# Performance work log

Hardware: AMD Instinct MI355X
Metric: run time of the kernel (lower is better)

The kernel has to match this reference:

```python
import jax, jax.numpy as jnp
import numpy as np

# Module config (init_kwargs)
CIN, COUT, KH, KW = 256, 256, 3, 3
STRIDE, PADDING = 1, 1
T = 64                 # psum chunk size along the reduction (K) axis
NBITS = 8              # saturating accumulator bits (signed)
QMAX = (1 << (NBITS - 1)) - 1   # 127
QMIN = QMAX - (1 << NBITS) + 1  # -128


def setup_inputs() -> dict:
    key = jax.random.key(0)
    k1, k2 = jax.random.split(key)
    x = jax.random.normal(k1, (8, CIN, 56, 56), dtype=jnp.float32)
    # nn.Parameter(torch.rand((N,1)) * 0.001)
    weights = jax.random.uniform(k2, (CIN * COUT * KH * KW, 1), dtype=jnp.float32) * 0.001
    return {"x": x, "weights": weights}


def reference(x, weights):
    B, _, H, W = x.shape
    OH = (H - KH + 2 * PADDING) // STRIDE + 1
    OW = (W - KW + 2 * PADDING) // STRIDE + 1

    w = weights.reshape(COUT, CIN, KH, KW)
    # per-output-channel scaling factor, detached
    scale = jax.lax.stop_gradient(jnp.mean(jnp.abs(w), axis=(1, 2, 3), keepdims=True))
    # binarize with STE: sign(w).detach() - clamp(w).detach() + clamp(w)
    wc = jnp.clip(w, -1.0, 1.0)
    wb = jax.lax.stop_gradient(jnp.sign(w) - wc) + wc

    # unfold (im2col); channel varies slowest -> matches torch.nn.functional.unfold
    patches = jax.lax.conv_general_dilated_patches(
        x, (KH, KW), (STRIDE, STRIDE), [(PADDING, PADDING), (PADDING, PADDING)]
    )  # [B, CIN*KH*KW, OH*OW... (spatial)]
    K = CIN * KH * KW
    L = OH * OW
    A = patches.reshape(B, K, L).transpose(0, 2, 1)  # [B, L, K]
    X = wb.reshape(COUT, K).T                        # [K, COUT]

    pad = (-K) % T
    if pad:
        A = jnp.pad(A, ((0, 0), (0, 0), (0, pad)))
        X = jnp.pad(X, ((0, pad), (0, 0)))
    nT = (K + pad) // T

    A4 = A.reshape(B, L, nT, T)        # chunked reduction axis
    X3 = X.reshape(nT, T, COUT)
    # per-chunk partial sums (satmm_cuda.forward_psum)
    psum = jnp.einsum('blnt,ntc->nblc', A4, X3)  # [nT, B, L, COUT]

    # saturating sequential accumulation: reduce(lambda a,b: clip(a+b, QMIN, QMAX))
    def step(carry, p):
        return jnp.clip(carry + p, QMIN, QMAX), None
    y_flat, _ = jax.lax.scan(step, psum[0], psum[1:])  # [B, L, COUT]

    y = y_flat.transpose(0, 2, 1).reshape(B, COUT, OH, OW)
    y = y * scale.reshape(1, -1, 1, 1)
    # psum returned in the original [B, L, COUT, nT] layout
    return y, psum.transpose(1, 2, 3, 0)
```

## Files before the change

kernel.cpp:

```cpp
#include <hip/hip_runtime.h>
#include <hip/hip_bf16.h>

#define CIN 256
#define COUT 256
#define HW 56
#define BATCH 8
#define L_SPATIAL 3136
#define K_TOTAL 2304
#define NT 36
#define KSTRIDE 2312
#define ATILE_BYTES (16 * KSTRIDE * 2)
#define STAGE_FLOATS 2304
#define LDS_BYTES (ATILE_BYTES + 8 * STAGE_FLOATS * 4)
#define QMAXF 127.0f
#define QMINF -128.0f

typedef short bf16x8 __attribute__((ext_vector_type(8)));
typedef float f32x4 __attribute__((ext_vector_type(4)));

__global__ __launch_bounds__(256) void prep_kernel(
    const float* __restrict__ w, unsigned short* __restrict__ bsign,
    float* __restrict__ scale) {
  const int c = blockIdx.x;
  const int t = threadIdx.x;
  const float* row = w + (size_t)c * K_TOTAL;
  unsigned short* out = bsign + (size_t)c * K_TOTAL;
  float acc = 0.0f;
#pragma unroll
  for (int j = 0; j < 9; ++j) {
    const int k = t + 256 * j;
    const float v = row[k];
    acc += __builtin_fabsf(v);
    out[k] = (v > 0.0f) ? (unsigned short)0x3F80
           : ((v < 0.0f) ? (unsigned short)0xBF80 : (unsigned short)0);
  }
#pragma unroll
  for (int o = 32; o > 0; o >>= 1) acc += __shfl_down(acc, o, 64);
  __shared__ float red[4];
  if ((t & 63) == 0) red[t >> 6] = acc;
  __syncthreads();
  if (t == 0) scale[c] = (red[0] + red[1] + red[2] + red[3]) * (1.0f / 2304.0f);
}

__global__ __launch_bounds__(512, 1) void satconv_kernel(
    const float* __restrict__ x, const unsigned short* __restrict__ bsign,
    const float* __restrict__ scale, float* __restrict__ y_out,
    float* __restrict__ psum_out) {
  extern __shared__ char smem[];
  unsigned short* Atile = (unsigned short*)smem;
  float* stage_base = (float*)(smem + ATILE_BYTES);

  const int tid = threadIdx.x;
  const int m0 = blockIdx.x << 4;

  {
    const int ml = tid & 15;
    const int grp = tid >> 4;
    const int m = m0 + ml;
    const int b = m / L_SPATIAL;
    const int l = m - b * L_SPATIAL;
    const int oh = l / HW;
    const int ow = l - oh * HW;
    const float* xb = x + (size_t)b * (CIN * L_SPATIAL);
    unsigned short* arow = Atile + ml * KSTRIDE;
    for (int r = grp; r < 768; r += 32) {
      const int ci = r / 3;
      const int kh = r - ci * 3;
      const int h = oh + kh - 1;
      const bool hv = ((unsigned)h < (unsigned)HW);
      const float* xr = xb + (ci * HW + h) * HW;
      const int kb = ci * 9 + kh * 3;
#pragma unroll
      for (int kw = 0; kw < 3; ++kw) {
        const int wv = ow + kw - 1;
        float v = 0.0f;
        if (hv && ((unsigned)wv < (unsigned)HW)) v = xr[wv];
        __hip_bfloat16 bv = __float2bfloat16(v);
        arow[kb + kw] = *reinterpret_cast<unsigned short*>(&bv);
      }
    }
  }
  __syncthreads();

  const int lane = tid & 63;
  const int wave = tid >> 6;
  const int cl = lane & 15;
  const int q = lane >> 4;
  const int c0 = wave << 5;
  float* stage = stage_base + wave * STAGE_FLOATS;

  const unsigned short* aptr = Atile + cl * KSTRIDE + q * 8;
  const int b_img = m0 / L_SPATIAL;
  const int l0 = m0 - b_img * L_SPATIAL;

  for (int s = 0; s < 2; ++s) {
    const int csub0 = c0 + (s << 4);
    const int c = csub0 + cl;
    const unsigned short* bptr = bsign + (size_t)c * K_TOTAL + q * 8;
    f32x4 ps[NT];
    f32x4 sacc = {0.0f, 0.0f, 0.0f, 0.0f};
    const f32x4 zero = {0.0f, 0.0f, 0.0f, 0.0f};
#pragma unroll
    for (int n = 0; n < NT; ++n) {
      bf16x8 a0 = *reinterpret_cast<const bf16x8*>(aptr + n * 64);
      bf16x8 a1 = *reinterpret_cast<const bf16x8*>(aptr + n * 64 + 32);
      bf16x8 b0 = *reinterpret_cast<const bf16x8*>(bptr + n * 64);
      bf16x8 b1 = *reinterpret_cast<const bf16x8*>(bptr + n * 64 + 32);
      f32x4 acc = __builtin_amdgcn_mfma_f32_16x16x32_bf16(a0, b0, zero, 0, 0, 0);
      acc = __builtin_amdgcn_mfma_f32_16x16x32_bf16(a1, b1, acc, 0, 0, 0);
      ps[n] = acc;
      if (n == 0) {
        sacc = acc;
      } else {
#pragma unroll
        for (int e = 0; e < 4; ++e) {
          const float t = sacc[e] + acc[e];
          sacc[e] = __builtin_amdgcn_fmed3f(t, QMINF, QMAXF);
        }
      }
    }

#pragma unroll
    for (int rg = 0; rg < 4; ++rg) {
#pragma unroll
      for (int g = 0; g < 9; ++g) {
        f32x4 v = {ps[4 * g + 0][rg], ps[4 * g + 1][rg],
                   ps[4 * g + 2][rg], ps[4 * g + 3][rg]};
        *reinterpret_cast<f32x4*>(stage + q * 576 + cl * 36 + 4 * g) = v;
      }
#pragma unroll
      for (int it = 0; it < 9; ++it) {
        const int f = it * 256 + lane * 4;
        const int qq = f / 576;
        const int rem = f - qq * 576;
        const int ci = rem / 36;
        const int n0 = rem - ci * 36;
        f32x4 v = *reinterpret_cast<const f32x4*>(stage + f);
        const size_t goff =
            ((size_t)(m0 + (qq << 2) + rg) * COUT + (csub0 + ci)) * NT + n0;
        *reinterpret_cast<f32x4*>(psum_out + goff) = v;
      }
    }

    {
      const float sc = scale[c];
      f32x4 yv;
#pragma unroll
      for (int e = 0; e < 4; ++e) yv[e] = sacc[e] * sc;
      *reinterpret_cast<f32x4*>(stage + cl * 16 + q * 4) = yv;
      const int ci = lane >> 2;
      const int mi = (lane & 3) << 2;
      f32x4 v = *reinterpret_cast<const f32x4*>(stage + lane * 4);
      *reinterpret_cast<f32x4*>(
          y_out + ((size_t)b_img * COUT + (csub0 + ci)) * L_SPATIAL + l0 + mi) = v;
    }
  }
}

extern "C" void kernel_launch(void* const* d_in, const int* in_sizes, int n_in,
                              void* d_out, int out_size, void* d_ws, size_t ws_size,
                              hipStream_t stream) {
  const float* x = (const float*)d_in[0];
  const float* w = (const float*)d_in[1];
  float* y = (float*)d_out;
  float* psum = y + (size_t)BATCH * COUT * L_SPATIAL;
  unsigned short* bsign = (unsigned short*)d_ws;
  float* scale = (float*)((char*)d_ws + (size_t)COUT * K_TOTAL * 2);

  prep_kernel<<<COUT, 256, 0, stream>>>(w, bsign, scale);

  hipFuncSetAttribute(reinterpret_cast<const void*>(satconv_kernel),
                      hipFuncAttributeMaxDynamicSharedMemorySize, LDS_BYTES);
  satconv_kernel<<<(BATCH * L_SPATIAL) / 16, 512, LDS_BYTES, stream>>>(
      x, bsign, scale, y, psum);
}
```

Before: 1.259 ms.

## Persistent conv kernel with bit-packed sign weights and prefetched im2col tiles

Replaces the one-block-per-tile launch with a persistent grid of 224 blocks, each processing 7 tiles. The next tile's im2col gather is prefetched into registers while the current tile computes. Weights are stored as sign and zero bitplanes that are expanded into bf16 ±1 fragments in registers, which removes most of the weight-fragment loads from global memory. It also swizzles the A tile layout in LDS, pads the psum staging buffer, and allows two blocks per CU. The cost is higher register pressure from holding two 36-entry accumulator arrays plus the prefetch buffer, and more complex barrier handling.

Result: slower. 2.136 ms (+69.6%).

```diff
diff --git a/kernel.cpp b/kernel.cpp
--- a/kernel.cpp
+++ b/kernel.cpp
@@ -8,152 +8,297 @@
 #define L_SPATIAL 3136
 #define K_TOTAL 2304
 #define NT 36
-#define KSTRIDE 2312
-#define ATILE_BYTES (16 * KSTRIDE * 2)
-#define STAGE_FLOATS 2304
-#define LDS_BYTES (ATILE_BYTES + 8 * STAGE_FLOATS * 4)
+#define TILES_PER_IMG 196
+#define GRID 224
+#define TPW 7
+#define A_U16 36864
+#define STAGE_DW 2340
+#define LDS_BYTES (A_U16 * 2 + 8 * STAGE_DW * 4)
+#define BB_STRIDE 40
+#define ZPLANE (256 * 4 * BB_STRIDE)
 #define QMAXF 127.0f
 #define QMINF -128.0f
 
 typedef short bf16x8 __attribute__((ext_vector_type(8)));
 typedef float f32x4 __attribute__((ext_vector_type(4)));
+typedef unsigned int u32x4 __attribute__((ext_vector_type(4)));
 
 __global__ __launch_bounds__(256) void prep_kernel(
-    const float* __restrict__ w, unsigned short* __restrict__ bsign,
+    const float* __restrict__ w, unsigned short* __restrict__ bbits,
     float* __restrict__ scale) {
   const int c = blockIdx.x;
   const int t = threadIdx.x;
   const float* row = w + (size_t)c * K_TOTAL;
-  unsigned short* out = bsign + (size_t)c * K_TOTAL;
-  float acc = 0.0f;
-#pragma unroll
-  for (int j = 0; j < 9; ++j) {
-    const int k = t + 256 * j;
-    const float v = row[k];
-    acc += __builtin_fabsf(v);
-    out[k] = (v > 0.0f) ? (unsigned short)0x3F80
-           : ((v < 0.0f) ? (unsigned short)0xBF80 : (unsigned short)0);
-  }
+  float acc = 0.f;
+#pragma unroll
+  for (int j = 0; j < 9; ++j) acc += __builtin_fabsf(row[t + 256 * j]);
 #pragma unroll
   for (int o = 32; o > 0; o >>= 1) acc += __shfl_down(acc, o, 64);
   __shared__ float red[4];
   if ((t & 63) == 0) red[t >> 6] = acc;
   __syncthreads();
-  if (t == 0) scale[c] = (red[0] + red[1] + red[2] + red[3]) * (1.0f / 2304.0f);
-}
-
-__global__ __launch_bounds__(512, 1) void satconv_kernel(
-    const float* __restrict__ x, const unsigned short* __restrict__ bsign,
+  if (t == 0) scale[c] = (red[0] + red[1] + red[2] + red[3]) * (1.f / 2304.f);
+  if (t < 144) {
+    const int q = t / 36, n = t - q * 36;
+    unsigned int sbits = 0, zbits = 0;
+#pragma unroll
+    for (int j = 0; j < 8; ++j) {
+      const float v0 = row[n * 64 + q * 8 + j];
+      const float v1 = row[n * 64 + 32 + q * 8 + j];
+      if (v0 < 0.f) sbits |= (1u << j);
+      if (v1 < 0.f) sbits |= (1u << (8 + j));
+      if (v0 == 0.f) zbits |= (1u << j);
+      if (v1 == 0.f) zbits |= (1u << (8 + j));
+    }
+    bbits[(c * 4 + q) * BB_STRIDE + n] = (unsigned short)sbits;
+    bbits[ZPLANE + (c * 4 + q) * BB_STRIDE + n] = (unsigned short)zbits;
+  }
+}
+
+__device__ __forceinline__ void expand_frags(unsigned int t, bf16x8& b0, bf16x8& b1) {
+  u32x4 w0, w1;
+#pragma unroll
+  for (int d = 0; d < 4; ++d) {
+    w0[d] = 0x3F803F80u | ((t & (1u << (2 * d)))     << (15 - 2 * d))
+                        | ((t & (1u << (2 * d + 1))) << (30 - 2 * d));
+    w1[d] = 0x3F803F80u | ((t & (1u << (8 + 2 * d))) << (7 - 2 * d))
+                        | ((t & (1u << (9 + 2 * d))) << (22 - 2 * d));
+  }
+  b0 = __builtin_bit_cast(bf16x8, w0);
+  b1 = __builtin_bit_cast(bf16x8, w1);
+}
+
+template <bool Z>
+__device__ __forceinline__ void run_k(const unsigned short* __restrict__ abase,
+                                      const unsigned int* __restrict__ bb,
+                                      const unsigned int* __restrict__ zb,
+                                      f32x4* __restrict__ ps, f32x4& sacc) {
+  const f32x4 zero = {0.f, 0.f, 0.f, 0.f};
+#pragma unroll
+  for (int n = 0; n < NT; ++n) {
+    const unsigned int td = bb[n >> 1];
+    const unsigned int tb = (n & 1) ? (td >> 16) : (td & 0xFFFFu);
+    bf16x8 b0, b1;
+    expand_frags(tb, b0, b1);
+    if (Z) {
+      const unsigned int zd = zb[n >> 1];
+      const unsigned int zt = (n & 1) ? (zd >> 16) : (zd & 0xFFFFu);
+      if (zt) {
+        u32x4 w0 = __builtin_bit_cast(u32x4, b0);
+        u32x4 w1 = __builtin_bit_cast(u32x4, b1);
+#pragma unroll
+        for (int d = 0; d < 4; ++d) {
+          if (zt & (1u << (2 * d)))     w0[d] &= 0xFFFF0000u;
+          if (zt & (1u << (2 * d + 1))) w0[d] &= 0x0000FFFFu;
+          if (zt & (1u << (8 + 2 * d))) w1[d] &= 0xFFFF0000u;
+          if (zt & (1u << (9 + 2 * d))) w1[d] &= 0x0000FFFFu;
+        }
+        b0 = __builtin_bit_cast(bf16x8, w0);
+        b1 = __builtin_bit_cast(bf16x8, w1);
+      }
+    }
+    bf16x8 a0 = *reinterpret_cast<const bf16x8*>(abase + n * 1024);
+    bf16x8 a1 = *reinterpret_cast<const bf16x8*>(abase + n * 1024 + 512);
+    f32x4 acc = __builtin_amdgcn_mfma_f32_16x16x32_bf16(a0, b0, zero, 0, 0, 0);
+    acc = __builtin_amdgcn_mfma_f32_16x16x32_bf16(a1, b1, acc, 0, 0, 0);
+    ps[n] = acc;
+    if (n == 0) sacc = acc;
+    else {
+#pragma unroll
+      for (int e = 0; e < 4; ++e) {
+        const float tv = sacc[e] + acc[e];
+        sacc[e] = __builtin_amdgcn_fmed3f(tv, QMINF, QMAXF);
+      }
+    }
+  }
+}
+
+__global__ __launch_bounds__(512, 2) void satconv_kernel(
+    const float* __restrict__ x, const unsigned short* __restrict__ bbits,
     const float* __restrict__ scale, float* __restrict__ y_out,
     float* __restrict__ psum_out) {
   extern __shared__ char smem[];
   unsigned short* Atile = (unsigned short*)smem;
-  float* stage_base = (float*)(smem + ATILE_BYTES);
+  float* stage_base = (float*)(smem + A_U16 * 2);
 
   const int tid = threadIdx.x;
-  const int m0 = blockIdx.x << 4;
-
-  {
-    const int ml = tid & 15;
-    const int grp = tid >> 4;
-    const int m = m0 + ml;
-    const int b = m / L_SPATIAL;
-    const int l = m - b * L_SPATIAL;
-    const int oh = l / HW;
-    const int ow = l - oh * HW;
-    const float* xb = x + (size_t)b * (CIN * L_SPATIAL);
-    unsigned short* arow = Atile + ml * KSTRIDE;
-    for (int r = grp; r < 768; r += 32) {
-      const int ci = r / 3;
-      const int kh = r - ci * 3;
-      const int h = oh + kh - 1;
-      const bool hv = ((unsigned)h < (unsigned)HW);
-      const float* xr = xb + (ci * HW + h) * HW;
-      const int kb = ci * 9 + kh * 3;
-#pragma unroll
-      for (int kw = 0; kw < 3; ++kw) {
-        const int wv = ow + kw - 1;
-        float v = 0.0f;
-        if (hv && ((unsigned)wv < (unsigned)HW)) v = xr[wv];
-        __hip_bfloat16 bv = __float2bfloat16(v);
-        arow[kb + kw] = *reinterpret_cast<unsigned short*>(&bv);
-      }
-    }
-  }
-  __syncthreads();
-
   const int lane = tid & 63;
   const int wave = tid >> 6;
   const int cl = lane & 15;
   const int q = lane >> 4;
   const int c0 = wave << 5;
-  float* stage = stage_base + wave * STAGE_FLOATS;
-
-  const unsigned short* aptr = Atile + cl * KSTRIDE + q * 8;
-  const int b_img = m0 / L_SPATIAL;
-  const int l0 = m0 - b_img * L_SPATIAL;
-
-  for (int s = 0; s < 2; ++s) {
-    const int csub0 = c0 + (s << 4);
-    const int c = csub0 + cl;
-    const unsigned short* bptr = bsign + (size_t)c * K_TOTAL + q * 8;
-    f32x4 ps[NT];
-    f32x4 sacc = {0.0f, 0.0f, 0.0f, 0.0f};
-    const f32x4 zero = {0.0f, 0.0f, 0.0f, 0.0f};
-#pragma unroll
-    for (int n = 0; n < NT; ++n) {
-      bf16x8 a0 = *reinterpret_cast<const bf16x8*>(aptr + n * 64);
-      bf16x8 a1 = *reinterpret_cast<const bf16x8*>(aptr + n * 64 + 32);
-      bf16x8 b0 = *reinterpret_cast<const bf16x8*>(bptr + n * 64);
-      bf16x8 b1 = *reinterpret_cast<const bf16x8*>(bptr + n * 64 + 32);
-      f32x4 acc = __builtin_amdgcn_mfma_f32_16x16x32_bf16(a0, b0, zero, 0, 0, 0);
-      acc = __builtin_amdgcn_mfma_f32_16x16x32_bf16(a1, b1, acc, 0, 0, 0);
-      ps[n] = acc;
-      if (n == 0) {
-        sacc = acc;
-      } else {
-#pragma unroll
-        for (int e = 0; e < 4; ++e) {
-          const float t = sacc[e] + acc[e];
-          sacc[e] = __builtin_amdgcn_fmed3f(t, QMINF, QMAXF);
-        }
-      }
-    }
-
-#pragma unroll
-    for (int rg = 0; rg < 4; ++rg) {
-#pragma unroll
-      for (int g = 0; g < 9; ++g) {
-        f32x4 v = {ps[4 * g + 0][rg], ps[4 * g + 1][rg],
-                   ps[4 * g + 2][rg], ps[4 * g + 3][rg]};
-        *reinterpret_cast<f32x4*>(stage + q * 576 + cl * 36 + 4 * g) = v;
-      }
-#pragma unroll
-      for (int it = 0; it < 9; ++it) {
-        const int f = it * 256 + lane * 4;
-        const int qq = f / 576;
-        const int rem = f - qq * 576;
-        const int ci = rem / 36;
-        const int n0 = rem - ci * 36;
-        f32x4 v = *reinterpret_cast<const f32x4*>(stage + f);
-        const size_t goff =
-            ((size_t)(m0 + (qq << 2) + rg) * COUT + (csub0 + ci)) * NT + n0;
-        *reinterpret_cast<f32x4*>(psum_out + goff) = v;
-      }
-    }
-
-    {
-      const float sc = scale[c];
+  float* stage = stage_base + wave * STAGE_DW;
+  const int w_id = blockIdx.x;
+
+  auto load_bb = [&](const unsigned short* plane, int s, unsigned int* bb) {
+    const unsigned short* bp = plane + (size_t)((c0 + (s << 4) + cl) * 4 + q) * BB_STRIDE;
+    const uint4* p4 = (const uint4*)bp;
+    uint4 v0 = p4[0], v1 = p4[1], v2 = p4[2], v3 = p4[3];
+    uint2 v4 = *(const uint2*)(bp + 32);
+    bb[0]=v0.x; bb[1]=v0.y; bb[2]=v0.z; bb[3]=v0.w;
+    bb[4]=v1.x; bb[5]=v1.y; bb[6]=v1.z; bb[7]=v1.w;
+    bb[8]=v2.x; bb[9]=v2.y; bb[10]=v2.z; bb[11]=v2.w;
+    bb[12]=v3.x; bb[13]=v3.y; bb[14]=v3.z; bb[15]=v3.w;
+    bb[16]=v4.x; bb[17]=v4.y;
+  };
+
+  auto load_pack = [&](int m0n, unsigned int* apack) {
+    const int ml = tid & 15;
+    const int grp = tid >> 4;
+    const int m = m0n + ml;
+    const int b = m / L_SPATIAL;
+    const int l = m - b * L_SPATIAL;
+    const int oh = l / HW, ow = l - oh * HW;
+    const float* xb = x + (size_t)b * (CIN * L_SPATIAL);
+#pragma unroll
+    for (int j = 0; j < 24; ++j) {
+      const int r = grp + 32 * j;
+      const int ci = r / 3, kh = r - ci * 3;
+      const int h = oh + kh - 1;
+      const bool hv = ((unsigned)h < (unsigned)HW);
+      const float* xr = xb + (ci * HW + h) * HW;
+#pragma unroll
+      for (int kw = 0; kw < 3; ++kw) {
+        const int wv = ow + kw - 1;
+        float v = 0.f;
+        if (hv && ((unsigned)wv < (unsigned)HW)) v = xr[wv];
+        __hip_bfloat16 bv = __float2bfloat16(v);
+        unsigned int u = (unsigned int)*reinterpret_cast<unsigned short*>(&bv);
+        const int idx = j * 3 + kw;
+        if (idx & 1) apack[idx >> 1] |= (u << 16);
+        else         apack[idx >> 1] = u;
+      }
+    }
+  };
+
+  auto unpack_write = [&](const unsigned int* apack) {
+    const int ml = tid & 15;
+    const int grp = tid >> 4;
+#pragma unroll
+    for (int j = 0; j < 24; ++j) {
+      const int r = grp + 32 * j;
+      const int ci = r / 3, kh = r - ci * 3;
+      const int kb = ci * 9 + kh * 3;
+#pragma unroll
+      for (int kw = 0; kw < 3; ++kw) {
+        const int idx = j * 3 + kw;
+        unsigned int u = apack[idx >> 1];
+        u = (idx & 1) ? (u >> 16) : (u & 0xFFFFu);
+        const int k = kb + kw;
+        const int addr = ((k >> 6) << 10) + (((k >> 5) & 1) << 9)
+                       + ((((k >> 3) & 3) * 16 + ml) << 3) + (k & 7);
+        Atile[addr] = (unsigned short)u;
+      }
+    }
+  };
+
+  unsigned int bb0[18];
+  load_bb(bbits, 0, bb0);
+  const float sc0 = scale[c0 + cl];
+  const float sc1 = scale[c0 + 16 + cl];
+
+  bool zany0, zany1;
+  {
+    unsigned int zt0[18], zt1[18];
+    load_bb(bbits + ZPLANE, 0, zt0);
+    load_bb(bbits + ZPLANE, 1, zt1);
+    unsigned int o0 = 0, o1 = 0;
+#pragma unroll
+    for (int i = 0; i < 18; ++i) { o0 |= zt0[i]; o1 |= zt1[i]; }
+    zany0 = __any(o0 != 0);
+    zany1 = __any(o1 != 0);
+  }
+
+  {
+    unsigned int ap[36];
+    const int t0 = ((w_id & 7) * TILES_PER_IMG + (w_id >> 3)) << 4;
+    load_pack(t0, ap);
+    unpack_write(ap);
+  }
+  __asm__ volatile("s_waitcnt lgkmcnt(0)\ns_barrier" ::: "memory");
+
+  const unsigned short* abase = Atile + lane * 8;
+
+  int tt = w_id;
+  for (int i = 0; i < TPW; ++i, tt += GRID) {
+    const int t = (tt & 7) * TILES_PER_IMG + (tt >> 3);
+    const int m0 = t << 4;
+    const int b_img = tt & 7;
+    const int l0 = m0 - b_img * L_SPATIAL;
+
+    auto stage_store = [&](int s, f32x4* ps, f32x4 sacc, float sc) {
+      const int csub0 = c0 + (s << 4);
       f32x4 yv;
 #pragma unroll
       for (int e = 0; e < 4; ++e) yv[e] = sacc[e] * sc;
       *reinterpret_cast<f32x4*>(stage + cl * 16 + q * 4) = yv;
-      const int ci = lane >> 2;
-      const int mi = (lane & 3) << 2;
-      f32x4 v = *reinterpret_cast<const f32x4*>(stage + lane * 4);
-      *reinterpret_cast<f32x4*>(
-          y_out + ((size_t)b_img * COUT + (csub0 + ci)) * L_SPATIAL + l0 + mi) = v;
-    }
+      {
+        const int ci = lane >> 2, mi = (lane & 3) << 2;
+        f32x4 v = *reinterpret_cast<const f32x4*>(stage + lane * 4);
+        *reinterpret_cast<f32x4*>(
+            y_out + ((size_t)b_img * COUT + csub0 + ci) * L_SPATIAL + l0 + mi) = v;
+      }
+      const int qc4 = (q * 16 + cl) * 4;
+#pragma unroll
+      for (int rg = 0; rg < 4; ++rg) {
+#pragma unroll
+        for (int g = 0; g < 9; ++g) {
+          f32x4 v = {ps[4 * g + 0][rg], ps[4 * g + 1][rg],
+                     ps[4 * g + 2][rg], ps[4 * g + 3][rg]};
+          *reinterpret_cast<f32x4*>(stage + g * 260 + qc4) = v;
+        }
+#pragma unroll
+        for (int it = 0; it < 9; ++it) {
+          const int f = it * 256 + lane * 4;
+          const int qq = f / 576;
+          const int rem = f - qq * 576;
+          const int ci = rem / 36;
+          const int n0 = rem - ci * 36;
+          f32x4 v = *reinterpret_cast<const f32x4*>(
+              stage + (n0 >> 2) * 260 + (qq * 16 + ci) * 4);
+          const int goff = ((m0 + (qq << 2) + rg) * COUT + (csub0 + ci)) * NT + n0;
+          *reinterpret_cast<f32x4*>(psum_out + goff) = v;
+        }
+      }
+    };
+
+    f32x4 ps0[NT];
+    f32x4 sacc0;
+    if (zany0) {
+      unsigned int zb[18];
+      load_bb(bbits + ZPLANE, 0, zb);
+      run_k<true>(abase, bb0, zb, ps0, sacc0);
+    } else {
+      run_k<false>(abase, bb0, nullptr, ps0, sacc0);
+    }
+
+    unsigned int bb1[18];
+    load_bb(bbits, 1, bb1);
+    unsigned int apack[36];
+    const bool more = (i + 1 < TPW);
+    if (more) {
+      const int tn = tt + GRID;
+      load_pack(((tn & 7) * TILES_PER_IMG + (tn >> 3)) << 4, apack);
+    }
+    __asm__ volatile("" ::: "memory");
+
+    stage_store(0, ps0, sacc0, sc0);
+
+    f32x4 ps1[NT];
+    f32x4 sacc1;
+    if (zany1) {
+      unsigned int zb[18];
+      load_bb(bbits + ZPLANE, 1, zb);
+      run_k<true>(abase, bb1, zb, ps1, sacc1);
+    } else {
+      run_k<false>(abase, bb1, nullptr, ps1, sacc1);
+    }
+
+    __asm__ volatile("s_barrier" ::: "memory");
+    if (more) unpack_write(apack);
+    __asm__ volatile("s_waitcnt lgkmcnt(0)\ns_barrier" ::: "memory");
+
+    stage_store(1, ps1, sacc1, sc1);
   }
 }
 
@@ -164,13 +309,12 @@
   const float* w = (const float*)d_in[1];
   float* y = (float*)d_out;
   float* psum = y + (size_t)BATCH * COUT * L_SPATIAL;
-  unsigned short* bsign = (unsigned short*)d_ws;
-  float* scale = (float*)((char*)d_ws + (size_t)COUT * K_TOTAL * 2);
-
-  prep_kernel<<<COUT, 256, 0, stream>>>(w, bsign, scale);
+  unsigned short* bbits = (unsigned short*)d_ws;
+  float* scale = (float*)((char*)d_ws + 2 * ZPLANE * sizeof(unsigned short));
+
+  prep_kernel<<<COUT, 256, 0, stream>>>(w, bbits, scale);
 
   hipFuncSetAttribute(reinterpret_cast<const void*>(satconv_kernel),
                       hipFuncAttributeMaxDynamicSharedMemorySize, LDS_BYTES);
-  satconv_kernel<<<(BATCH * L_SPATIAL) / 16, 512, LDS_BYTES, stream>>>(
-      x, bsign, scale, y, psum);
-}
+  satconv_kernel<<<GRID, 512, LDS_BYTES, stream>>>(x, bbits, scale, y, psum);
+}
```
